# Kernel tuning notes

Measured on AMD Instinct MI355X. Metric: run time of the kernel, lower is better.

## Reference

```python
import jax, jax.numpy as jnp
import numpy as np

# Module hyperparameters (init_kwargs)
FS = 30.0          # sampling rate (Hz)
HIGH_PASS = 40.0   # bpm
LOW_PASS = 250.0   # bpm
DELTA_T = 300      # crop length (samples)
K = 64             # crops per (batch, channel)
B, C, T = 256, 16, 9000

NBINS = DELTA_T // 2 + 1  # rfft bins
# freqs = linspace(0, Fs/2, NBINS); band mask is static given shapes
_freqs = np.linspace(0.0, FS / 2.0, NBINS)
MASK_IDX = np.where((_freqs >= HIGH_PASS / 60.0) & (_freqs <= LOW_PASS / 60.0))[0]


def setup_inputs() -> dict:
    key = jax.random.key(0)
    k1, k2 = jax.random.split(key)
    inp = jax.random.normal(k1, (B, C, T), dtype=jnp.float32)
    # random temporal offsets, one per (b, c, k) crop
    offsets = jax.random.randint(k2, (B, C, K), 0, T - DELTA_T + 1, dtype=jnp.int32)
    return {"input": inp, "offsets": offsets}


def reference(input, offsets):
    # Batched gather of all random crops: [B, C, K, DELTA_T]
    t_idx = offsets[..., None] + jnp.arange(DELTA_T, dtype=jnp.int32)  # [B,C,K,dt]
    crops = jnp.take_along_axis(input[:, :, None, :], t_idx, axis=-1)
    # Remove per-crop mean
    crops = crops - jnp.mean(crops, axis=-1, keepdims=True)
    # rFFT with 'forward' norm (divide by n), power spectrum
    spec = jnp.fft.rfft(crops, axis=-1, norm='forward')   # [B,C,K,NBINS] complex
    power = spec.real ** 2 + spec.imag ** 2               # [B,C,K,NBINS]
    # Keep only the heart-rate band (static index set), normalize to unit sum
    power = power[..., MASK_IDX]                          # [B,C,K,F_band]
    power = power / jnp.sum(power, axis=-1, keepdims=True)
    return power
```

## Files before the change

kernel.cpp:

```cpp
#include <hip/hip_runtime.h>
#include <math.h>

#define TT 9000
#define DT 300
#define KK 64
#define NB 35
#define KMIN 7
#define NCH 4096
#define NPAIR (KK * NB)


typedef __bf16 bf16;
typedef __attribute__((ext_vector_type(8))) __bf16 bf16x8;
typedef __attribute__((ext_vector_type(4))) float f32x4;

#define NFRAG_ELEMS (10 * 6 * 64 * 8)

__global__ void build_w(bf16* __restrict__ tab) {
    int i = blockIdx.x * blockDim.x + threadIdx.x;
    if (i >= NFRAG_ELEMS) return;
    int j    = i & 7;
    int l    = (i >> 3) & 63;
    int f    = i >> 9;
    int nt   = f % 6;
    int ks   = f / 6;
    int quad = l >> 4;
    int c    = l & 15;
    int k    = ks * 32 + quad * 8 + j;
    int jf   = (nt % 3) * 16 + c;
    float v = 0.0f;
    if (jf <= NB - 1 && k < DT) {
        int bin = jf + KMIN;
        int ph  = (bin * k) % DT;
        float ang = 0.02094395102393195f * (float)ph;
        v = (nt >= 3) ? sinf(ang) : cosf(ang);
    }
    tab[i] = (bf16)v;
}

__global__ __launch_bounds__(256, 4) void st_mfma(
        const float* __restrict__ input,
        const int*   __restrict__ offsets,
        const bf16*  __restrict__ tab,
        float*       __restrict__ out) {
    __shared__ __align__(16) float sig[TT + 32];
    __shared__ int offs[KK];

    const int bc  = blockIdx.x;
    const int tid = threadIdx.x;

    const float4* src = (const float4*)(input + (size_t)bc * TT);
    float4* dst = (float4*)sig;
#pragma unroll
    for (int i = 0; i < 9; ++i) {
        int idx = tid + i * 256;
        if (idx < TT / 4) dst[idx] = src[idx];
    }
    if (tid < 32) sig[TT + tid] = 0.0f;
    if (tid < KK) offs[tid] = offsets[bc * KK + tid];
    __syncthreads();

    const int w    = tid >> 6;
    const int lane = tid & 63;
    const int quad = lane >> 4;
    const int c    = lane & 15;

    const int   off = offs[w * 16 + c];
    const float* sp = sig + off + quad * 8;

    const bf16x8* wt = (const bf16x8*)tab;

    f32x4 acc[6];
#pragma unroll
    for (int nt = 0; nt < 6; ++nt) acc[nt] = (f32x4){0.f, 0.f, 0.f, 0.f};

    float  a_f[8];
    bf16x8 bb[6];
#pragma unroll
    for (int j = 0; j < 8; ++j) a_f[j] = sp[j];
#pragma unroll
    for (int nt = 0; nt < 6; ++nt) bb[nt] = wt[nt * 64 + lane];

#pragma unroll
    for (int ks = 0; ks < 10; ++ks) {
        bf16x8 a;
#pragma unroll
        for (int j = 0; j < 8; ++j) a[j] = (bf16)a_f[j];

        float  a_n[8];
        bf16x8 bn[6];
        if (ks < 9) {
            const float* p = sp + (ks + 1) * 32;
#pragma unroll
            for (int j = 0; j < 8; ++j) a_n[j] = p[j];
#pragma unroll
            for (int nt = 0; nt < 6; ++nt) bn[nt] = wt[((ks + 1) * 6 + nt) * 64 + lane];
        }

#pragma unroll
        for (int nt = 0; nt < 6; ++nt)
            acc[nt] = __builtin_amdgcn_mfma_f32_16x16x32_bf16(a, bb[nt], acc[nt], 0, 0, 0);

        if (ks < 9) {
#pragma unroll
            for (int j = 0; j < 8; ++j) a_f[j] = a_n[j];
#pragma unroll
            for (int nt = 0; nt < 6; ++nt) bb[nt] = bn[nt];
        }
    }

    float* o = out + (size_t)bc * NPAIR;
#pragma unroll
    for (int r = 0; r < 4; ++r) {
        float p0 = acc[0][r] * acc[0][r] + acc[3][r] * acc[3][r];
        float p1 = acc[1][r] * acc[1][r] + acc[4][r] * acc[4][r];
        float p2 = acc[2][r] * acc[2][r] + acc[5][r] * acc[5][r];
        float s = p0 + p1 + ((c <= 2) ? p2 : 0.0f);
#pragma unroll
        for (int d = 1; d < 16; d <<= 1) s += __shfl_xor(s, d, 64);
        float rinv = 1.0f / s;
        int crop = w * 16 + quad * 4 + r;
        float* oc = o + crop * NB;
        oc[c] = p0 * rinv;
        oc[16 + c] = p1 * rinv;
        if (c <= 2) oc[32 + c] = p2 * rinv;
    }
}

extern "C" void kernel_launch(void* const* d_in, const int* in_sizes, int n_in,
                              void* d_out, int out_size, void* d_ws, size_t ws_size,
                              hipStream_t stream) {
    const float* input   = (const float*)d_in[0];
    const int*   offsets = (const int*)d_in[1];
    float*       out     = (float*)d_out;
    bf16*        tab     = (bf16*)d_ws;

    build_w<<<(NFRAG_ELEMS + 255) / 256, 256, 0, stream>>>(tab);
    st_mfma<<<NCH, 256, 0, stream>>>(input, offsets, tab, out);
}
```

Measured before the change: 239.8 us.

## Gather crops directly into bf16 LDS rows and split MFMA work across six waves

Instead of copying the whole 9000-sample channel into LDS as float, the kernel gathers only the 64 crop windows from global memory, converts them to bf16, and stores them in padded LDS rows. The block grows to 384 threads, with six waves split by crop half and frequency tile. Each wave keeps its 10 k-steps of cosine/sine weights in registers and reads A fragments from LDS. Row sums are combined across waves through a small shared array, and the reciprocal uses the rcp intrinsic. The aim is to cut global and LDS traffic and to raise parallelism, at the cost of overlapping scalar global loads, an extra barrier and higher register pressure.

```diff
diff --git a/kernel.cpp b/kernel.cpp
--- a/kernel.cpp
+++ b/kernel.cpp
@@ -12,6 +12,7 @@
 
 typedef __bf16 bf16;
 typedef __attribute__((ext_vector_type(8))) __bf16 bf16x8;
+typedef __attribute__((ext_vector_type(4))) __bf16 bf16x4;
 typedef __attribute__((ext_vector_type(4))) float f32x4;
 
 #define NFRAG_ELEMS (10 * 6 * 64 * 8)
@@ -38,92 +39,102 @@
     tab[i] = (bf16)v;
 }
 
-__global__ __launch_bounds__(256, 4) void st_mfma(
+#define ROWB 656
+
+__global__ __launch_bounds__(384, 3) void st_mfma(
         const float* __restrict__ input,
         const int*   __restrict__ offsets,
         const bf16*  __restrict__ tab,
         float*       __restrict__ out) {
-    __shared__ __align__(16) float sig[TT + 32];
+    __shared__ __align__(16) unsigned char cb[KK * ROWB];
+    __shared__ __align__(16) float part[KK][4];
     __shared__ int offs[KK];
 
     const int bc  = blockIdx.x;
     const int tid = threadIdx.x;
 
-    const float4* src = (const float4*)(input + (size_t)bc * TT);
-    float4* dst = (float4*)sig;
-#pragma unroll
-    for (int i = 0; i < 9; ++i) {
-        int idx = tid + i * 256;
-        if (idx < TT / 4) dst[idx] = src[idx];
-    }
-    if (tid < 32) sig[TT + tid] = 0.0f;
     if (tid < KK) offs[tid] = offsets[bc * KK + tid];
     __syncthreads();
 
-    const int w    = tid >> 6;
+    const float* chan = input + (size_t)bc * TT;
+#pragma unroll 4
+    for (int i = 0; i < 14; ++i) {
+        int n = tid + i * 384;
+        if (n < KK * 80) {
+            int r = n / 80;
+            int p = n - r * 80;
+            float f0 = 0.f, f1 = 0.f, f2 = 0.f, f3 = 0.f;
+            if (p < 75) {
+                const float* gp = chan + offs[r] + p * 4;
+                f0 = gp[0]; f1 = gp[1]; f2 = gp[2]; f3 = gp[3];
+            }
+            bf16x4 v;
+            v[0] = (bf16)f0; v[1] = (bf16)f1; v[2] = (bf16)f2; v[3] = (bf16)f3;
+            *(bf16x4*)(cb + r * ROWB + p * 8) = v;
+        }
+    }
+
+    const int wid  = tid >> 6;
     const int lane = tid & 63;
+    const int mg   = wid & 1;
+    const int pg   = wid >> 1;
+
+    bf16x8 wc[10], ws[10];
+#pragma unroll
+    for (int ks = 0; ks < 10; ++ks) {
+        wc[ks] = *(const bf16x8*)(tab + (size_t)((ks * 6 + pg    ) * 64 + lane) * 8);
+        ws[ks] = *(const bf16x8*)(tab + (size_t)((ks * 6 + pg + 3) * 64 + lane) * 8);
+    }
+
+    __syncthreads();
+
     const int quad = lane >> 4;
     const int c    = lane & 15;
 
-    const int   off = offs[w * 16 + c];
-    const float* sp = sig + off + quad * 8;
+    const unsigned char* a0p = cb + (mg * 32 + c) * ROWB + quad * 16;
+    const unsigned char* a1p = a0p + 16 * ROWB;
 
-    const bf16x8* wt = (const bf16x8*)tab;
-
-    f32x4 acc[6];
-#pragma unroll
-    for (int nt = 0; nt < 6; ++nt) acc[nt] = (f32x4){0.f, 0.f, 0.f, 0.f};
-
-    float  a_f[8];
-    bf16x8 bb[6];
-#pragma unroll
-    for (int j = 0; j < 8; ++j) a_f[j] = sp[j];
-#pragma unroll
-    for (int nt = 0; nt < 6; ++nt) bb[nt] = wt[nt * 64 + lane];
+    f32x4 acc_c0 = {0.f,0.f,0.f,0.f}, acc_s0 = {0.f,0.f,0.f,0.f};
+    f32x4 acc_c1 = {0.f,0.f,0.f,0.f}, acc_s1 = {0.f,0.f,0.f,0.f};
 
 #pragma unroll
     for (int ks = 0; ks < 10; ++ks) {
-        bf16x8 a;
+        bf16x8 a0 = *(const bf16x8*)(a0p + ks * 64);
+        bf16x8 a1 = *(const bf16x8*)(a1p + ks * 64);
+        acc_c0 = __builtin_amdgcn_mfma_f32_16x16x32_bf16(a0, wc[ks], acc_c0, 0, 0, 0);
+        acc_s0 = __builtin_amdgcn_mfma_f32_16x16x32_bf16(a0, ws[ks], acc_s0, 0, 0, 0);
+        acc_c1 = __builtin_amdgcn_mfma_f32_16x16x32_bf16(a1, wc[ks], acc_c1, 0, 0, 0);
+        acc_s1 = __builtin_amdgcn_mfma_f32_16x16x32_bf16(a1, ws[ks], acc_s1, 0, 0, 0);
+    }
+
+    float pv[2][4];
 #pragma unroll
-        for (int j = 0; j < 8; ++j) a[j] = (bf16)a_f[j];
-
-        float  a_n[8];
-        bf16x8 bn[6];
-        if (ks < 9) {
-            const float* p = sp + (ks + 1) * 32;
+    for (int m = 0; m < 2; ++m) {
 #pragma unroll
-            for (int j = 0; j < 8; ++j) a_n[j] = p[j];
+        for (int r = 0; r < 4; ++r) {
+            float cv = m ? acc_c1[r] : acc_c0[r];
+            float sv = m ? acc_s1[r] : acc_s0[r];
+            float p  = cv * cv + sv * sv;
+            pv[m][r] = p;
+            float s = p;
 #pragma unroll
-            for (int nt = 0; nt < 6; ++nt) bn[nt] = wt[((ks + 1) * 6 + nt) * 64 + lane];
-        }
-
-#pragma unroll
-        for (int nt = 0; nt < 6; ++nt)
-            acc[nt] = __builtin_amdgcn_mfma_f32_16x16x32_bf16(a, bb[nt], acc[nt], 0, 0, 0);
-
-        if (ks < 9) {
-#pragma unroll
-            for (int j = 0; j < 8; ++j) a_f[j] = a_n[j];
-#pragma unroll
-            for (int nt = 0; nt < 6; ++nt) bb[nt] = bn[nt];
+            for (int d = 1; d < 16; d <<= 1) s += __shfl_xor(s, d, 64);
+            if (c == 0) part[mg * 32 + m * 16 + quad * 4 + r][pg] = s;
         }
     }
+    __syncthreads();
 
-    float* o = out + (size_t)bc * NPAIR;
+    float* ob = out + (size_t)bc * NPAIR;
 #pragma unroll
-    for (int r = 0; r < 4; ++r) {
-        float p0 = acc[0][r] * acc[0][r] + acc[3][r] * acc[3][r];
-        float p1 = acc[1][r] * acc[1][r] + acc[4][r] * acc[4][r];
-        float p2 = acc[2][r] * acc[2][r] + acc[5][r] * acc[5][r];
-        float s = p0 + p1 + ((c <= 2) ? p2 : 0.0f);
+    for (int m = 0; m < 2; ++m) {
 #pragma unroll
-        for (int d = 1; d < 16; d <<= 1) s += __shfl_xor(s, d, 64);
-        float rinv = 1.0f / s;
-        int crop = w * 16 + quad * 4 + r;
-        float* oc = o + crop * NB;
-        oc[c] = p0 * rinv;
-        oc[16 + c] = p1 * rinv;
-        if (c <= 2) oc[32 + c] = p2 * rinv;
+        for (int r = 0; r < 4; ++r) {
+            int crop = mg * 32 + m * 16 + quad * 4 + r;
+            f32x4 t = *(const f32x4*)part[crop];
+            float rinv = __builtin_amdgcn_rcpf(t[0] + t[1] + t[2]);
+            if (pg < 2 || c < 3)
+                ob[crop * 35 + pg * 16 + c] = pv[m][r] * rinv;
+        }
     }
 }
 
@@ -136,5 +147,5 @@
     bf16*        tab     = (bf16*)d_ws;
 
     build_w<<<(NFRAG_ELEMS + 255) / 256, 256, 0, stream>>>(tab);
-    st_mfma<<<NCH, 256, 0, stream>>>(input, offsets, tab, out);
+    st_mfma<<<NCH, 384, 0, stream>>>(input, offsets, tab, out);
 }
```

Result: slower. 293.8 us (+22.5%).

## Stage signal in LDS as bf16 and build MFMA operands via alignbit

Applied to the files above, without the earlier changes.

Converts the signal to bf16 once while staging it into shared memory, which halves LDS use (about 18 KB instead of 36 KB) so launch_bounds can be raised to 8 blocks per CU. The A fragments are built from five dword LDS loads per k-step, with alignbit fixing odd offsets, replacing eight float loads and conversions. The explicit software prefetch of A and B fragments is dropped, so load scheduling is left to the compiler. The risk is less latency hiding within each wave, traded against more waves resident per CU.

```diff
diff --git a/kernel.cpp b/kernel.cpp
--- a/kernel.cpp
+++ b/kernel.cpp
@@ -12,6 +12,7 @@
 
 typedef __bf16 bf16;
 typedef __attribute__((ext_vector_type(8))) __bf16 bf16x8;
+typedef __attribute__((ext_vector_type(4))) __bf16 bf16x4;
 typedef __attribute__((ext_vector_type(4))) float f32x4;
 
 #define NFRAG_ELEMS (10 * 6 * 64 * 8)
@@ -38,25 +39,31 @@
     tab[i] = (bf16)v;
 }
 
-__global__ __launch_bounds__(256, 4) void st_mfma(
+#define SPAD 9024
+
+__global__ __launch_bounds__(256, 8) void st_mfma(
         const float* __restrict__ input,
         const int*   __restrict__ offsets,
         const bf16*  __restrict__ tab,
         float*       __restrict__ out) {
-    __shared__ __align__(16) float sig[TT + 32];
+    __shared__ __align__(16) bf16 sig[SPAD];
     __shared__ int offs[KK];
 
     const int bc  = blockIdx.x;
     const int tid = threadIdx.x;
 
     const float4* src = (const float4*)(input + (size_t)bc * TT);
-    float4* dst = (float4*)sig;
 #pragma unroll
     for (int i = 0; i < 9; ++i) {
         int idx = tid + i * 256;
-        if (idx < TT / 4) dst[idx] = src[idx];
+        if (idx < TT / 4) {
+            float4 v = src[idx];
+            bf16x4 b;
+            b[0] = (bf16)v.x; b[1] = (bf16)v.y; b[2] = (bf16)v.z; b[3] = (bf16)v.w;
+            *(bf16x4*)(sig + idx * 4) = b;
+        }
     }
-    if (tid < 32) sig[TT + tid] = 0.0f;
+    if (tid < SPAD - TT) sig[TT + tid] = (bf16)0.0f;
     if (tid < KK) offs[tid] = offsets[bc * KK + tid];
     __syncthreads();
 
@@ -65,8 +72,10 @@
     const int quad = lane >> 4;
     const int c    = lane & 15;
 
-    const int   off = offs[w * 16 + c];
-    const float* sp = sig + off + quad * 8;
+    const int off = offs[w * 16 + c];
+    const int d0  = (off + quad * 8) >> 1;
+    const unsigned sh = (unsigned)((off & 1) << 4);
+    const int* ip = (const int*)sig;
 
     const bf16x8* wt = (const bf16x8*)tab;
 
@@ -74,39 +83,21 @@
 #pragma unroll
     for (int nt = 0; nt < 6; ++nt) acc[nt] = (f32x4){0.f, 0.f, 0.f, 0.f};
 
-    float  a_f[8];
-    bf16x8 bb[6];
-#pragma unroll
-    for (int j = 0; j < 8; ++j) a_f[j] = sp[j];
-#pragma unroll
-    for (int nt = 0; nt < 6; ++nt) bb[nt] = wt[nt * 64 + lane];
-
 #pragma unroll
     for (int ks = 0; ks < 10; ++ks) {
-        bf16x8 a;
-#pragma unroll
-        for (int j = 0; j < 8; ++j) a[j] = (bf16)a_f[j];
-
-        float  a_n[8];
-        bf16x8 bn[6];
-        if (ks < 9) {
-            const float* p = sp + (ks + 1) * 32;
-#pragma unroll
-            for (int j = 0; j < 8; ++j) a_n[j] = p[j];
-#pragma unroll
-            for (int nt = 0; nt < 6; ++nt) bn[nt] = wt[((ks + 1) * 6 + nt) * 64 + lane];
-        }
+        const int db = d0 + ks * 16;
+        int dw0 = ip[db + 0], dw1 = ip[db + 1], dw2 = ip[db + 2],
+            dw3 = ip[db + 3], dw4 = ip[db + 4];
+        union { unsigned u[4]; bf16x8 v; } a;
+        a.u[0] = __builtin_amdgcn_alignbit((unsigned)dw1, (unsigned)dw0, sh);
+        a.u[1] = __builtin_amdgcn_alignbit((unsigned)dw2, (unsigned)dw1, sh);
+        a.u[2] = __builtin_amdgcn_alignbit((unsigned)dw3, (unsigned)dw2, sh);
+        a.u[3] = __builtin_amdgcn_alignbit((unsigned)dw4, (unsigned)dw3, sh);
 
 #pragma unroll
         for (int nt = 0; nt < 6; ++nt)
-            acc[nt] = __builtin_amdgcn_mfma_f32_16x16x32_bf16(a, bb[nt], acc[nt], 0, 0, 0);
-
-        if (ks < 9) {
-#pragma unroll
-            for (int j = 0; j < 8; ++j) a_f[j] = a_n[j];
-#pragma unroll
-            for (int nt = 0; nt < 6; ++nt) bb[nt] = bn[nt];
-        }
+            acc[nt] = __builtin_amdgcn_mfma_f32_16x16x32_bf16(
+                a.v, wt[(ks * 6 + nt) * 64 + lane], acc[nt], 0, 0, 0);
     }
 
     float* o = out + (size_t)bc * NPAIR;
```

Measured after the change: 251.2 us. 1.05x slower.
